# Optimization experiments

Measured on AMD Instinct MI355X. Metric: run time of the kernel, lower is better.

Reference implementation:

```python
import jax, jax.numpy as jnp
import numpy as np

K = 121          # kernel_size
C = 3            # channels
PAD = (K - 1) // 2  # 60, replicate padding so output matches input spatial size


def setup_inputs() -> dict:
    key = jax.random.key(0)
    k1, k2 = jax.random.split(key)
    x = jax.random.normal(k1, (8, C, 512, 512), dtype=jnp.float32)
    sigma = jax.random.uniform(k2, (), dtype=jnp.float32)
    return {"x": x, "sigma": sigma}


def _gaussian_kernel(sigma):
    # sigma -> sigma*8 + 16, variance = sigma**2 (as in torch forward)
    s = sigma * 8.0 + 16.0
    variance = s * s
    coord = jnp.arange(K, dtype=jnp.float32) - (K - 1) / 2.0  # centered coords
    diff = -(coord[:, None] ** 2 + coord[None, :] ** 2)       # [K,K], -((x-m)^2+(y-m)^2)
    kern = jnp.exp(diff / (2.0 * variance))
    # the 1/(2*pi*variance) prefactor cancels under normalization
    kern = kern / jnp.sum(kern)
    return kern


def reference(x, sigma):
    kern = _gaussian_kernel(sigma)
    # depthwise weights: [out_ch=C, in_ch/groups=1, K, K]
    w = jnp.broadcast_to(kern[None, None, :, :], (C, 1, K, K))
    # replicate padding (torch 'replicate' == jnp 'edge')
    xp = jnp.pad(x, ((0, 0), (0, 0), (PAD, PAD), (PAD, PAD)), mode="edge")
    out = jax.lax.conv_general_dilated(
        xp, w,
        window_strides=(1, 1),
        padding="VALID",
        dimension_numbers=("NCHW", "OIHW", "NCHW"),
        feature_group_count=C,
    )
    return out
```

## Files before the change

### kernel.cpp

```cpp
#include <hip/hip_runtime.h>


#define HH      512
#define WW      512
#define PLANE   (512 * 512)
#define NIMG    24
#define HPG_ROW 984

__device__ __forceinline__ void make_weights(const float* __restrict__ sigma,
                                             float* __restrict__ wlds, int tid) {
    const float s = sigma[0] * 8.0f + 16.0f;
    const float inv2v = 1.0f / (2.0f * s * s);
    float sum = 0.0f;
    #pragma unroll
    for (int k = 0; k <= 120; ++k) {
        const float c = (float)k - 60.0f;
        sum += __expf(-c * c * inv2v);
    }
    if (tid < 128) {
        float g = 0.0f;
        if (tid < 121) {
            const float c = (float)tid - 60.0f;
            g = __expf(-c * c * inv2v);
        }
        wlds[tid] = g / sum;
    }
}

#define V_OCT(CUR, NXT, KO)                                               \
    { *(float4*)&wq[0] = *(const float4*)&wlds[(KO) * 8];                 \
      *(float4*)&wq[4] = *(const float4*)&wlds[(KO) * 8 + 4];             \
      _Pragma("unroll")                                                   \
      for (int ki = 0; ki < 8; ++ki) {                                    \
          int rr = r0 - 52 + (KO) * 8 + ki;                               \
          rr = rr < 0 ? 0 : (rr > HH - 1 ? HH - 1 : rr);                  \
          NXT[ki] = *(const float2*)&src[(size_t)rr * WW];                \
          const float wk = wq[ki];                                        \
          _Pragma("unroll")                                               \
          for (int j = 0; j < 8; ++j) {                                   \
              const int idx = ki + j;                                     \
              const float2 v = (idx < 8) ? CUR[idx] : NXT[idx - 8];       \
              vac[j].x += wk * v.x; vac[j].y += wk * v.y;                 \
          }                                                               \
      }                                                                   \
    }

#define LOADG(DST, G)                                                     \
    { *(float4*)&DST[0] = *(const float4*)&bs[(G) * 12];                  \
      *(float4*)&DST[4] = *(const float4*)&bs[(G) * 12 + 4]; }

#define H_OCT2(A0, A1, A2, A3, B0, B1, B2, B3, KO)                        \
    { LOADG(A3, L + (KO) + 3)                                             \
      LOADG(B3, L + 32 + (KO) + 3)                                        \
      *(float4*)&wq[0] = *(const float4*)&wlds[(KO) * 8];                 \
      *(float4*)&wq[4] = *(const float4*)&wlds[(KO) * 8 + 4];             \
      _Pragma("unroll")                                                   \
      for (int ki = 0; ki < 8; ++ki) {                                    \
          const float wk = wq[ki];                                        \
          _Pragma("unroll")                                               \
          for (int j = 0; j < 8; ++j) {                                   \
              const int idx = ki + j;                                     \
              const float vA = (idx < 8) ? A0[idx]                        \
                             : (idx < 16) ? A1[idx - 8] : A2[idx - 16];   \
              const float vB = (idx < 8) ? B0[idx]                        \
                             : (idx < 16) ? B1[idx - 8] : B2[idx - 16];   \
              accA[j] += wk * vA;                                         \
              accB[j] += wk * vB;                                         \
          }                                                               \
      }                                                                   \
    }

__global__ __launch_bounds__(256, 4) void blur_fused(
        const float* __restrict__ x, const float* __restrict__ sigma,
        float* __restrict__ out) {
    __shared__ float sm[8 * HPG_ROW];
    __shared__ float wlds[128];
    const int tid = threadIdx.x;

    const int lid   = blockIdx.x + gridDim.x * blockIdx.y;
    const int tile  = (lid & 7) * 192 + (lid >> 3);
    const int r0    = (tile & 63) * 8;
    const int plane = tile >> 6;

    const int c0 = tid * 2;
    const float* __restrict__ src = x + (size_t)plane * PLANE + c0;

    float2 wa[8], wb[8], vac[8];
    float  wq[8];
    #pragma unroll
    for (int m = 0; m < 8; ++m) {
        int rr = r0 - 60 + m;
        rr = rr < 0 ? 0 : rr;
        wa[m] = *(const float2*)&src[(size_t)rr * WW];
    }
    make_weights(sigma, wlds, tid);
    #pragma unroll
    for (int j = 0; j < 8; ++j) vac[j] = make_float2(0.f, 0.f);
    __syncthreads();

    #pragma unroll 1
    for (int ko = 0; ko < 16; ko += 2) {
        V_OCT(wa, wb, ko)
        V_OCT(wb, wa, ko + 1)
    }

    {
        const int p  = c0 + 60;
        const int la = (p >> 3) * 12 + (p & 7);
        #pragma unroll
        for (int j = 0; j < 8; ++j)
            *(float2*)&sm[j * HPG_ROW + la] = vac[j];
    }
    __syncthreads();

    if (tid < 144) {
        int p, srca;
        if (tid < 60)       { p = tid;       srca = 7 * 12 + 4;  }
        else if (tid < 136) { p = 512 + tid; srca = 71 * 12 + 3; }
        else                { p = 512 + tid; srca = -1;          }
        const int dsta = (p >> 3) * 12 + (p & 7);
        #pragma unroll
        for (int r = 0; r < 8; ++r)
            sm[r * HPG_ROW + dsta] = (srca < 0) ? 0.0f
                                                : sm[r * HPG_ROW + srca];
    }
    __syncthreads();

    const int r = tid >> 5;
    const int L = tid & 31;
    const float* __restrict__ bs = sm + r * HPG_ROW;

    float a0[8], a1[8], a2[8], a3[8];
    float b0[8], b1[8], b2[8], b3[8];
    float accA[8], accB[8];
    #pragma unroll
    for (int j = 0; j < 8; ++j) { accA[j] = 0.0f; accB[j] = 0.0f; }

    LOADG(a0, L)      LOADG(b0, L + 32)
    LOADG(a1, L + 1)  LOADG(b1, L + 33)
    LOADG(a2, L + 2)  LOADG(b2, L + 34)

    #pragma unroll 1
    for (int ko = 0; ko < 16; ko += 4) {
        H_OCT2(a0, a1, a2, a3, b0, b1, b2, b3, ko)
        H_OCT2(a1, a2, a3, a0, b1, b2, b3, b0, ko + 1)
        H_OCT2(a2, a3, a0, a1, b2, b3, b0, b1, ko + 2)
        H_OCT2(a3, a0, a1, a2, b3, b0, b1, b2, ko + 3)
    }

    float* __restrict__ dst = out + (size_t)plane * PLANE
                                  + (size_t)(r0 + r) * WW + L * 8;
    *(float4*)(dst)        = make_float4(accA[0], accA[1], accA[2], accA[3]);
    *(float4*)(dst + 4)    = make_float4(accA[4], accA[5], accA[6], accA[7]);
    *(float4*)(dst + 256)  = make_float4(accB[0], accB[1], accB[2], accB[3]);
    *(float4*)(dst + 260)  = make_float4(accB[4], accB[5], accB[6], accB[7]);
}

extern "C" void kernel_launch(void* const* d_in, const int* in_sizes, int n_in,
                              void* d_out, int out_size, void* d_ws, size_t ws_size,
                              hipStream_t stream) {
    const float* x     = (const float*)d_in[0];
    const float* sigma = (const float*)d_in[1];
    float* out = (float*)d_out;
    blur_fused<<<dim3(HH / 8, NIMG), dim3(256), 0, stream>>>(x, sigma, out);
}
```

Measured before the change: 118.5 us.

## Swizzle LDS layout, move normalization to a wave reduce, raise occupancy

```diff
diff --git a/kernel.cpp b/kernel.cpp
--- a/kernel.cpp
+++ b/kernel.cpp
@@ -1,30 +1,29 @@
 #include <hip/hip_runtime.h>
 
 
-#define HH      512
-#define WW      512
-#define PLANE   (512 * 512)
-#define NIMG    24
-#define HPG_ROW 984
+#define HH    512
+#define WW    512
+#define PLANE (512 * 512)
+#define NIMG  24
+#define ROWF  672
 
 __device__ __forceinline__ void make_weights(const float* __restrict__ sigma,
                                              float* __restrict__ wlds, int tid) {
-    const float s = sigma[0] * 8.0f + 16.0f;
-    const float inv2v = 1.0f / (2.0f * s * s);
-    float sum = 0.0f;
-    #pragma unroll
-    for (int k = 0; k <= 120; ++k) {
-        const float c = (float)k - 60.0f;
-        sum += __expf(-c * c * inv2v);
-    }
     if (tid < 128) {
+        const float s = sigma[0] * 8.0f + 16.0f;
+        const float inv2v = 1.0f / (2.0f * s * s);
         float g = 0.0f;
         if (tid < 121) {
             const float c = (float)tid - 60.0f;
             g = __expf(-c * c * inv2v);
         }
-        wlds[tid] = g / sum;
+        wlds[tid] = g;
     }
+}
+
+__device__ __forceinline__ int swz_off(int col) {
+    const int u = col >> 2;
+    return ((u ^ ((u >> 3) & 7)) << 2) + (col & 3);
 }
 
 #define V_OCT(CUR, NXT, KO)                                               \
@@ -45,13 +44,17 @@
       }                                                                   \
     }
 
-#define LOADG(DST, G)                                                     \
-    { *(float4*)&DST[0] = *(const float4*)&bs[(G) * 12];                  \
-      *(float4*)&DST[4] = *(const float4*)&bs[(G) * 12 + 4]; }
+#define LOADG2(DA, DB, G)                                                 \
+    { const int u_  = 2 * (G);                                            \
+      const int o1_ = (u_ ^ ((u_ >> 3) & 7)) << 2;                        \
+      const int o2_ = o1_ ^ 4;                                            \
+      *(float4*)&DA[0] = *(const float4*)(bs + o1_);                      \
+      *(float4*)&DA[4] = *(const float4*)(bs + o2_);                      \
+      *(float4*)&DB[0] = *(const float4*)(bs + o1_ + 256);                \
+      *(float4*)&DB[4] = *(const float4*)(bs + o2_ + 256); }
 
 #define H_OCT2(A0, A1, A2, A3, B0, B1, B2, B3, KO)                        \
-    { LOADG(A3, L + (KO) + 3)                                             \
-      LOADG(B3, L + 32 + (KO) + 3)                                        \
+    { LOADG2(A3, B3, L + (KO) + 3)                                        \
       *(float4*)&wq[0] = *(const float4*)&wlds[(KO) * 8];                 \
       *(float4*)&wq[4] = *(const float4*)&wlds[(KO) * 8 + 4];             \
       _Pragma("unroll")                                                   \
@@ -70,10 +73,10 @@
       }                                                                   \
     }
 
-__global__ __launch_bounds__(256, 4) void blur_fused(
+__global__ __launch_bounds__(256, 6) void blur_fused(
         const float* __restrict__ x, const float* __restrict__ sigma,
         float* __restrict__ out) {
-    __shared__ float sm[8 * HPG_ROW];
+    __shared__ float sm[8 * ROWF];
     __shared__ float wlds[128];
     const int tid = threadIdx.x;
 
@@ -98,6 +101,12 @@
     for (int j = 0; j < 8; ++j) vac[j] = make_float2(0.f, 0.f);
     __syncthreads();
 
+    const int lane = tid & 63;
+    float s_sum = wlds[lane] + wlds[lane + 64];
+    #pragma unroll
+    for (int o = 32; o >= 1; o >>= 1) s_sum += __shfl_xor(s_sum, o);
+    const float inv_s2 = 1.0f / (s_sum * s_sum);
+
     #pragma unroll 1
     for (int ko = 0; ko < 16; ko += 2) {
         V_OCT(wa, wb, ko)
@@ -105,30 +114,31 @@
     }
 
     {
-        const int p  = c0 + 60;
-        const int la = (p >> 3) * 12 + (p & 7);
+        const int off = swz_off(c0 + 60);
         #pragma unroll
         for (int j = 0; j < 8; ++j)
-            *(float2*)&sm[j * HPG_ROW + la] = vac[j];
+            *(float2*)&sm[j * ROWF + off] = vac[j];
     }
     __syncthreads();
 
-    if (tid < 144) {
-        int p, srca;
-        if (tid < 60)       { p = tid;       srca = 7 * 12 + 4;  }
-        else if (tid < 136) { p = 512 + tid; srca = 71 * 12 + 3; }
-        else                { p = 512 + tid; srca = -1;          }
-        const int dsta = (p >> 3) * 12 + (p & 7);
+    if (tid < 36) {
+        const int p = (tid < 15) ? tid * 4
+                    : (tid < 34) ? 572 + (tid - 15) * 4
+                                 : 648 + (tid - 34) * 4;
+        const int u   = p >> 2;
+        const int off = (u ^ ((u >> 3) & 7)) << 2;
+        const int soff = (tid < 15) ? swz_off(60) : swz_off(571);
         #pragma unroll
-        for (int r = 0; r < 8; ++r)
-            sm[r * HPG_ROW + dsta] = (srca < 0) ? 0.0f
-                                                : sm[r * HPG_ROW + srca];
+        for (int r8 = 0; r8 < 8; ++r8) {
+            const float v = (tid < 34) ? sm[r8 * ROWF + soff] : 0.0f;
+            *(float4*)&sm[r8 * ROWF + off] = make_float4(v, v, v, v);
+        }
     }
     __syncthreads();
 
     const int r = tid >> 5;
     const int L = tid & 31;
-    const float* __restrict__ bs = sm + r * HPG_ROW;
+    const float* __restrict__ bs = sm + r * ROWF;
 
     float a0[8], a1[8], a2[8], a3[8];
     float b0[8], b1[8], b2[8], b3[8];
@@ -136,9 +146,9 @@
     #pragma unroll
     for (int j = 0; j < 8; ++j) { accA[j] = 0.0f; accB[j] = 0.0f; }
 
-    LOADG(a0, L)      LOADG(b0, L + 32)
-    LOADG(a1, L + 1)  LOADG(b1, L + 33)
-    LOADG(a2, L + 2)  LOADG(b2, L + 34)
+    LOADG2(a0, b0, L)
+    LOADG2(a1, b1, L + 1)
+    LOADG2(a2, b2, L + 2)
 
     #pragma unroll 1
     for (int ko = 0; ko < 16; ko += 4) {
@@ -150,10 +160,15 @@
 
     float* __restrict__ dst = out + (size_t)plane * PLANE
                                   + (size_t)(r0 + r) * WW + L * 8;
-    *(float4*)(dst)        = make_float4(accA[0], accA[1], accA[2], accA[3]);
-    *(float4*)(dst + 4)    = make_float4(accA[4], accA[5], accA[6], accA[7]);
-    *(float4*)(dst + 256)  = make_float4(accB[0], accB[1], accB[2], accB[3]);
-    *(float4*)(dst + 260)  = make_float4(accB[4], accB[5], accB[6], accB[7]);
+    const float k2 = inv_s2;
+    *(float4*)(dst)       = make_float4(accA[0] * k2, accA[1] * k2,
+                                        accA[2] * k2, accA[3] * k2);
+    *(float4*)(dst + 4)   = make_float4(accA[4] * k2, accA[5] * k2,
+                                        accA[6] * k2, accA[7] * k2);
+    *(float4*)(dst + 256) = make_float4(accB[0] * k2, accB[1] * k2,
+                                        accB[2] * k2, accB[3] * k2);
+    *(float4*)(dst + 260) = make_float4(accB[4] * k2, accB[5] * k2,
+                                        accB[6] * k2, accB[7] * k2);
 }
 
 extern "C" void kernel_launch(void* const* d_in, const int* in_sizes, int n_in,
```

After: 119.3 us. No clear change (+0.7%).
